# Optimization experiments

Hardware: AMD Instinct MI355X
Metric: run time of the kernel (lower is better)

## Reference

```python
import jax, jax.numpy as jnp
import numpy as np

D = 512          # sequence_dim
H = 8            # num_heads
DA = 64          # attn_dim per head
DV = 64          # linear_dim per head
NB = 4           # num_blocks
N = 1024         # max_seq_length + max_output_len + 1
B = 4
EPS = 1e-6


def setup_inputs() -> dict:
    key = jax.random.key(0)
    ks = jax.random.split(key, 8)
    sequence = jax.random.normal(ks[0], (B, N, D), dtype=jnp.float32)
    sequence_length = jax.random.randint(ks[1], (B,), 1, 1014)
    pos_embed = jax.random.normal(ks[2], (N, D), dtype=jnp.float32)  # nn.Embedding ~ N(0,1)
    w_uvqk = jax.random.normal(ks[3], (NB, D, 2 * H * DV + 2 * H * DA), dtype=jnp.float32) * 0.02
    w_o = jax.random.normal(ks[4], (NB, H * DV, D), dtype=jnp.float32) * 0.02
    b_o = jnp.zeros((NB, D), dtype=jnp.float32)
    ln1_g = jnp.ones((NB, D), dtype=jnp.float32)
    ln1_b = jnp.zeros((NB, D), dtype=jnp.float32)
    ln2_g = jnp.ones((NB, H * DV), dtype=jnp.float32)
    ln2_b = jnp.zeros((NB, H * DV), dtype=jnp.float32)
    pos_w = jax.random.normal(ks[5], (NB, 2 * N - 1), dtype=jnp.float32) * 0.02
    return {
        'sequence': sequence, 'sequence_length': sequence_length,
        'pos_embed': pos_embed, 'ln1_g': ln1_g, 'ln1_b': ln1_b,
        'w_uvqk': w_uvqk, 'ln2_g': ln2_g, 'ln2_b': ln2_b,
        'w_o': w_o, 'b_o': b_o, 'pos_w': pos_w,
    }


def _layer_norm(x, g, b):
    mu = jnp.mean(x, axis=-1, keepdims=True)
    var = jnp.mean(jnp.square(x - mu), axis=-1, keepdims=True)
    return (x - mu) * jax.lax.rsqrt(var + EPS) * g + b


def reference(sequence, sequence_length, pos_embed, ln1_g, ln1_b, w_uvqk,
              ln2_g, ln2_b, w_o, b_o, pos_w):
    # positional embedding + scale (inference: dropout = identity)
    x = sequence * jnp.asarray(np.sqrt(D), sequence.dtype) + pos_embed[None, :, :]
    # length mask (dense-padded equivalent of the jagged representation)
    mask = (jnp.arange(N)[None, :] < sequence_length[:, None]).astype(sequence.dtype)[..., None]
    x = x * mask
    # invalid_attn_mask = 1 - triu(ones, diag=1): causal incl. diagonal
    causal = jnp.tril(jnp.ones((N, N), sequence.dtype))
    # rel_pos_bias[i, j] = pos_w[j - i + N - 1]
    idx = jnp.arange(N)
    rel = idx[None, :] - idx[:, None] + (N - 1)  # (N, N) in [0, 2N-2]
    for l in range(NB):
        nx = _layer_norm(x, ln1_g[l], ln1_b[l])
        uvqk = jax.nn.silu(nx @ w_uvqk[l])  # (B, N, 2*H*DV + 2*H*DA)
        u, v, q, k = jnp.split(uvqk, [H * DV, 2 * H * DV, 2 * H * DV + H * DA], axis=-1)
        qh = q.reshape(x.shape[0], N, H, DA)
        kh = k.reshape(x.shape[0], N, H, DA)
        vh = v.reshape(x.shape[0], N, H, DV)
        qk = jnp.einsum('bnhd,bmhd->bhnm', qh, kh) + pos_w[l][rel][None, None]
        attn = jax.nn.silu(qk) * (causal / N)  # (B, H, N, N)
        av = jnp.einsum('bhnm,bmhd->bnhd', attn, vh).reshape(x.shape[0], N, H * DV)
        o_in = _layer_norm(av, ln2_g[l], ln2_b[l]) * u
        x = (x + o_in @ w_o[l] + b_o[l]) * mask  # mask = dense<->jagged roundtrip
    # output_embeddings[..., :D] then L2-normalize with clamped norm
    norm = jnp.linalg.norm(x, axis=-1, keepdims=True)
    return x / jnp.clip(norm, 1e-6, None)
```

## Files before the change

kernel.cpp:

```cpp
#include <hip/hip_runtime.h>
#include <math.h>
#include <stdint.h>

#define BB 4
#define NN 1024
#define DD 512
#define HH 8
#define ROWS (BB * NN)
#define NBL 4

typedef _Float16 h8 __attribute__((ext_vector_type(8)));
typedef _Float16 h4 __attribute__((ext_vector_type(4)));
typedef _Float16 h2 __attribute__((ext_vector_type(2)));
typedef float f4 __attribute__((ext_vector_type(4)));

__device__ __forceinline__ float fast_silu(float x) {
    float e = __builtin_amdgcn_exp2f(-1.4426950408889634f * x);
    return x * __builtin_amdgcn_rcpf(1.0f + e);
}

__device__ __forceinline__ void gl16(const void* gp, void* lp) {
    __builtin_amdgcn_global_load_lds(
        (const __attribute__((address_space(1))) uint32_t*)gp,
        (__attribute__((address_space(3))) uint32_t*)lp, 16, 0, 0);
}

__global__ __launch_bounds__(256) void k_transpose16(const float* __restrict__ wuvqk,
                                                     _Float16* __restrict__ wuT,
                                                     const float* __restrict__ wo,
                                                     _Float16* __restrict__ woT) {
    __shared__ _Float16 T[64][66];
    int z = blockIdx.z;
    const float* s; _Float16* d; int N;
    if (z < 4) { N = 2048; s = wuvqk + (size_t)z * 512 * 2048; d = wuT + (size_t)z * 2048 * 512; }
    else {
        if (blockIdx.x >= 8) return;
        N = 512; s = wo + (size_t)(z - 4) * 512 * 512; d = woT + (size_t)(z - 4) * 512 * 512;
    }
    int n0 = blockIdx.x << 6, k0 = blockIdx.y << 6;
    int tx = threadIdx.x & 63, ty = threadIdx.x >> 6;
    #pragma unroll
    for (int q = 0; q < 16; ++q)
        T[(q << 2) + ty][tx] = (_Float16)s[(size_t)(k0 + (q << 2) + ty) * N + n0 + tx];
    __syncthreads();
    #pragma unroll
    for (int q = 0; q < 16; ++q)
        d[(size_t)(n0 + (q << 2) + ty) * 512 + k0 + tx] = T[tx][(q << 2) + ty];
}

template<int INIT>
__global__ __launch_bounds__(256) void k_ln(const float* __restrict__ X,
                                            const float* __restrict__ X2,
                                            const float* __restrict__ X3,
                                            const float* __restrict__ seq,
                                            const float* __restrict__ pos,
                                            const int* __restrict__ slen,
                                            const float* __restrict__ g,
                                            const float* __restrict__ bt,
                                            _Float16* __restrict__ O,
                                            const _Float16* __restrict__ U,
                                            float* __restrict__ Xw) {
    __shared__ float sbuf[4];
    int row = blockIdx.x;
    int c = threadIdx.x << 1;
    float2 v;
    if (INIT) {
        int b = row >> 10, n = row & (NN - 1);
        float m = (n < slen[b]) ? 1.0f : 0.0f;
        float2 s2 = *(const float2*)&seq[(size_t)row * 512 + c];
        float2 p2 = *(const float2*)&pos[(size_t)n * 512 + c];
        const float SD = 22.627416997969522f;
        v.x = (s2.x * SD + p2.x) * m;
        v.y = (s2.y * SD + p2.y) * m;
        *(float2*)&Xw[(size_t)row * 512 + c] = v;
    } else {
        v = *(const float2*)&X[(size_t)row * 512 + c];
        int nn = row & 1023;
        if (X2 && nn >= 384) {
            float2 v2 = *(const float2*)&X2[(size_t)row * 512 + c];
            v.x += v2.x; v.y += v2.y;
        }
        if (X3 && nn >= 768) {
            float2 v3 = *(const float2*)&X3[(size_t)row * 512 + c];
            v.x += v3.x; v.y += v3.y;
        }
    }

    float s = v.x + v.y;
    #pragma unroll
    for (int off = 1; off < 64; off <<= 1) s += __shfl_xor(s, off);
    if ((threadIdx.x & 63) == 0) sbuf[threadIdx.x >> 6] = s;
    __syncthreads();
    s = sbuf[0] + sbuf[1] + sbuf[2] + sbuf[3];
    float mu = s * (1.0f / 512.0f);
    float dx = v.x - mu, dy = v.y - mu;
    float ss = dx * dx + dy * dy;
    __syncthreads();
    #pragma unroll
    for (int off = 1; off < 64; off <<= 1) ss += __shfl_xor(ss, off);
    if ((threadIdx.x & 63) == 0) sbuf[threadIdx.x >> 6] = ss;
    __syncthreads();
    ss = sbuf[0] + sbuf[1] + sbuf[2] + sbuf[3];
    float rs = rsqrtf(ss * (1.0f / 512.0f) + 1e-6f);

    float o0 = dx * rs * g[c] + bt[c];
    float o1 = dy * rs * g[c + 1] + bt[c + 1];
    if (U) {
        o0 *= (float)U[(size_t)row * 2048 + c];
        o1 *= (float)U[(size_t)row * 2048 + c + 1];
    }
    h2 o;
    o[0] = (_Float16)o0; o[1] = (_Float16)o1;
    *(h2*)&O[(size_t)row * 512 + c] = o;
}

template<int EPI, int BM, int BN, int WAVES, int WGR, int WGC>
__global__ __launch_bounds__(WAVES * 64) void k_gemm(const _Float16* __restrict__ A,
                                                     const _Float16* __restrict__ Bm,
                                                     int K, int Ncols,
                                                     _Float16* __restrict__ Cu,
                                                     _Float16* __restrict__ vT,
                                                     const float* __restrict__ bo,
                                                     const int* __restrict__ slen,
                                                     float* __restrict__ Xio) {
    constexpr int WR = BM / WGR / 16;
    constexpr int WC = BN / WGC / 16;
    constexpr int QA = BM * 8 / (WAVES * 64);
    constexpr int QB = BN * 8 / (WAVES * 64);
    __shared__ _Float16 As[2][BM * 64];
    __shared__ _Float16 Bs[2][BN * 64];
    int tid = threadIdx.x;
    int w = tid >> 6, lane = tid & 63;
    int t = lane & 15, gq = lane >> 4;
    int flat = blockIdx.y * gridDim.x + blockIdx.x;
    int cpx = (gridDim.x * gridDim.y) >> 3;
    int f2 = (flat & 7) * cpx + (flat >> 3);
    int bx = f2 % gridDim.x, by = f2 / gridDim.x;
    int row0 = by * BM, col0 = bx * BN;
    int wr = (w / WGC) * (BM / WGR), wc = (w % WGC) * (BN / WGC);

    f4 zero4 = {0.0f, 0.0f, 0.0f, 0.0f};
    f4 acc[WR][WC];
    #pragma unroll
    for (int i = 0; i < WR; ++i)
        #pragma unroll
        for (int j = 0; j < WC; ++j) acc[i][j] = zero4;

    auto stage = [&](int buf, int k0) {
        #pragma unroll
        for (int q = 0; q < QA; ++q) {
            int s = (q * WAVES + w) * 64 + lane;
            int r = s >> 3, cs = (s & 7) ^ (r & 7);
            gl16(A + (size_t)(row0 + r) * K + k0 + (cs << 3),
                 (char*)&As[buf][0] + (size_t)(q * WAVES + w) * 1024);
        }
        #pragma unroll
        for (int q = 0; q < QB; ++q) {
            int s = (q * WAVES + w) * 64 + lane;
            int r = s >> 3, cs = (s & 7) ^ (r & 7);
            gl16(Bm + (size_t)(col0 + r) * K + k0 + (cs << 3),
                 (char*)&Bs[buf][0] + (size_t)(q * WAVES + w) * 1024);
        }
    };

    stage(0, 0);
    int cur = 0;
    for (int k0 = 0; k0 < K; k0 += 64) {
        __syncthreads();
        if (k0 + 64 < K) stage(cur ^ 1, k0 + 64);
        h8 af[WR][2], bf[WC][2];
        #pragma unroll
        for (int i = 0; i < WR; ++i) {
            int rl = wr + (i << 4) + t;
            #pragma unroll
            for (int ks = 0; ks < 2; ++ks)
                af[i][ks] = *(const h8*)((const char*)&As[cur][0] + rl * 128 +
                                         (((gq + (ks << 2)) ^ (rl & 7)) << 4));
        }
        #pragma unroll
        for (int j = 0; j < WC; ++j) {
            int nl = wc + (j << 4) + t;
            #pragma unroll
            for (int ks = 0; ks < 2; ++ks)
                bf[j][ks] = *(const h8*)((const char*)&Bs[cur][0] + nl * 128 +
                                         (((gq + (ks << 2)) ^ (nl & 7)) << 4));
        }
        #pragma unroll
        for (int i = 0; i < WR; ++i)
            #pragma unroll
            for (int j = 0; j < WC; ++j) {
                acc[i][j] = __builtin_amdgcn_mfma_f32_16x16x32_f16(af[i][0], bf[j][0], acc[i][j], 0, 0, 0);
                acc[i][j] = __builtin_amdgcn_mfma_f32_16x16x32_f16(af[i][1], bf[j][1], acc[i][j], 0, 0, 0);
            }
        cur ^= 1;
    }

    #pragma unroll
    for (int i = 0; i < WR; ++i) {
        #pragma unroll
        for (int j = 0; j < WC; ++j) {
            int colf = col0 + wc + (j << 4) + t;
            int rowb = row0 + wr + (i << 4) + (gq << 2);
            if (EPI == 0) {
                if (colf >= 512 && colf < 1024) {
                    int b = rowb >> 10;
                    int hh = (colf - 512) >> 6, dd = (colf - 512) & 63;
                    h4 pk;
                    #pragma unroll
                    for (int rr = 0; rr < 4; ++rr) pk[rr] = (_Float16)fast_silu(acc[i][j][rr]);
                    size_t off = ((size_t)((b << 3) + hh) * 64 + dd) * 1024 + (rowb & 1023);
                    *(h4*)&vT[off] = pk;
                } else {
                    #pragma unroll
                    for (int rr = 0; rr < 4; ++rr)
                        Cu[(size_t)(rowb + rr) * 2048 + colf] = (_Float16)fast_silu(acc[i][j][rr]);
                }
            } else {
                int b = rowb >> 10;
                #pragma unroll
                for (int rr = 0; rr < 4; ++rr) {
                    int row = rowb + rr;
                    float m = ((row & 1023) < slen[b]) ? 1.0f : 0.0f;
                    size_t ix = (size_t)row * 512 + colf;
                    Xio[ix] = (Xio[ix] + acc[i][j][rr] + bo[colf]) * m;
                }
            }
        }
    }
}

__global__ __launch_bounds__(256) void k_attn(const _Float16* __restrict__ uvqk,
                                              const _Float16* __restrict__ vT,
                                              const float* __restrict__ posw,
                                              float* __restrict__ av0,
                                              float* __restrict__ av1,
                                              float* __restrict__ av2) {
    __shared__ _Float16 Ks[2][64 * 64];
    __shared__ _Float16 Vs[64 * 64];
    __shared__ _Float16 Ps[64 * 72];
    __shared__ float pws[2][128];
    int tid = threadIdx.x;
    int w = tid >> 6, lane = tid & 63;
    int t = lane & 15, gq = lane >> 4;
    int flat = blockIdx.x + 30 * (blockIdx.y + 8 * blockIdx.z);
    int f2 = (flat & 7) * 120 + (flat >> 3);
    int u = f2 % 30, h = (f2 / 30) & 7, b = f2 / 240;

    int nt, mlo, mhi;
    float* avout;
    if (u < 6) { nt = u; mlo = 0; mhi = nt; avout = av0; }
    else if (u < 18) {
        int p = u - 6; nt = 6 + (p >> 1);
        int c0 = (nt + 2) >> 1;
        if (p & 1) { mlo = c0; mhi = nt; avout = av1; }
        else       { mlo = 0;  mhi = c0 - 1; avout = av0; }
    } else {
        int p = u - 18; int third = p / 3; nt = 12 + third; int q3 = p - 3 * third;
        int c = nt + 1;
        int c1 = (c + 2) / 3, c2 = (2 * c + 2) / 3;
        if (q3 == 0)      { mlo = 0;  mhi = c1 - 1; avout = av0; }
        else if (q3 == 1) { mlo = c1; mhi = c2 - 1; avout = av1; }
        else              { mlo = c2; mhi = nt;     avout = av2; }
    }
    int n0 = nt << 6;

    const _Float16* qbase = uvqk + (size_t)b * NN * 2048 + 1024 + h * 64;
    const _Float16* kbase = uvqk + (size_t)b * NN * 2048 + 1536 + h * 64;
    const _Float16* vbase = vT + (size_t)((b << 3) + h) * 64 * 1024;

    #pragma unroll
    for (int q = 0; q < 2; ++q) {
        int s = (((w << 1) + q) << 6) + lane;
        int r = s >> 3, cs = (s & 7) ^ (r & 7);
        gl16(qbase + (size_t)(n0 + r) * 2048 + (cs << 3),
             (char*)&Ks[1][0] + (size_t)(((w << 1) + q) << 6) * 16);
        gl16(kbase + (size_t)((mlo << 6) + r) * 2048 + (cs << 3),
             (char*)&Ks[0][0] + (size_t)(((w << 1) + q) << 6) * 16);
    }
    if (tid < 128) pws[0][tid] = posw[(mlo << 6) - n0 + tid + 960];
    __syncthreads();

    h8 aq[2];
    {
        int rl = (w << 4) + t;
        #pragma unroll
        for (int ks = 0; ks < 2; ++ks)
            aq[ks] = *(const h8*)((const char*)&Ks[1][0] + rl * 128 +
                                  (((gq + (ks << 2)) ^ (rl & 7)) << 4));
    }
    asm volatile("s_waitcnt lgkmcnt(0)" ::: "memory");
    __builtin_amdgcn_sched_barrier(0);
    __syncthreads();

    f4 zero4 = {0.0f, 0.0f, 0.0f, 0.0f};
    f4 avacc[4];
    #pragma unroll
    for (int j = 0; j < 4; ++j) avacc[j] = zero4;

    int cur = 0;
    for (int mt = mlo; mt <= mhi; ++mt) {
        int m0 = mt << 6;
        #pragma unroll
        for (int q = 0; q < 2; ++q) {
            int s = (((w << 1) + q) << 6) + lane;
            int r = s >> 3, cs = (s & 7) ^ (r & 7);
            gl16(vbase + (size_t)r * 1024 + m0 + (cs << 3),
                 (char*)&Vs[0] + (size_t)(((w << 1) + q) << 6) * 16);
        }
        int mt2 = (mt < mhi) ? mt + 1 : mt;
        #pragma unroll
        for (int q = 0; q < 2; ++q) {
            int s = (((w << 1) + q) << 6) + lane;
            int r = s >> 3, cs = (s & 7) ^ (r & 7);
            gl16(kbase + (size_t)((mt2 << 6) + r) * 2048 + (cs << 3),
                 (char*)&Ks[cur ^ 1][0] + (size_t)(((w << 1) + q) << 6) * 16);
        }
        if (tid < 128) pws[cur ^ 1][tid] = posw[(mt2 << 6) - n0 + tid + 960];

        f4 sacc[4];
        __builtin_amdgcn_s_setprio(1);
        #pragma unroll
        for (int i = 0; i < 4; ++i) {
            f4 binit;
            #pragma unroll
            for (int rr = 0; rr < 4; ++rr)
                binit[rr] = pws[cur][63 + (i << 4) + (gq << 2) + rr - ((w << 4) + t)];
            int ml = (i << 4) + t;
            h8 ak0 = *(const h8*)((const char*)&Ks[cur][0] + ml * 128 + (((gq + 0) ^ (ml & 7)) << 4));
            h8 ak1 = *(const h8*)((const char*)&Ks[cur][0] + ml * 128 + (((gq + 4) ^ (ml & 7)) << 4));
            sacc[i] = __builtin_amdgcn_mfma_f32_16x16x32_f16(ak0, aq[0], binit, 0, 0, 0);
            sacc[i] = __builtin_amdgcn_mfma_f32_16x16x32_f16(ak1, aq[1], sacc[i], 0, 0, 0);
        }
        __builtin_amdgcn_s_setprio(0);
        int nabs = n0 + (w << 4) + t;
        #pragma unroll
        for (int i = 0; i < 4; ++i) {
            int mb = m0 + (i << 4) + (gq << 2);
            h4 pk;
            #pragma unroll
            for (int rr = 0; rr < 4; ++rr) {
                float p = (mb + rr <= nabs) ? fast_silu(sacc[i][rr]) : 0.0f;
                pk[rr] = (_Float16)p;
            }
            *(h4*)((char*)Ps + ((w << 4) + t) * 144 + (i << 5) + (gq << 3)) = pk;
        }
        asm volatile("s_waitcnt lgkmcnt(0)" ::: "memory");
        asm volatile("s_waitcnt vmcnt(2)" ::: "memory");
        __builtin_amdgcn_s_barrier();
        __builtin_amdgcn_s_setprio(1);
        #pragma unroll
        for (int ks = 0; ks < 2; ++ks) {
            h8 pa = *(const h8*)((const char*)Ps + ((w << 4) + t) * 144 + (ks << 6) + (gq << 4));
            #pragma unroll
            for (int jt = 0; jt < 4; ++jt) {
                int dl = (jt << 4) + t;
                h8 bv = *(const h8*)((const char*)&Vs[0] + dl * 128 +
                                     (((gq + (ks << 2)) ^ (dl & 7)) << 4));
                avacc[jt] = __builtin_amdgcn_mfma_f32_16x16x32_f16(pa, bv, avacc[jt], 0, 0, 0);
            }
        }
        __builtin_amdgcn_s_setprio(0);
        __syncthreads();
        cur ^= 1;
    }

    #pragma unroll
    for (int jt = 0; jt < 4; ++jt) {
        #pragma unroll
        for (int rr = 0; rr < 4; ++rr) {
            int n = n0 + (w << 4) + (gq << 2) + rr;
            int d = (jt << 4) + t;
            avout[(size_t)(b * NN + n) * 512 + h * 64 + d] = avacc[jt][rr] * (1.0f / 1024.0f);
        }
    }
}

__global__ __launch_bounds__(256) void k_norm(float* __restrict__ X) {
    __shared__ float sbuf[4];
    int row = blockIdx.x;
    int c = threadIdx.x << 1;
    float2 v = *(const float2*)&X[(size_t)row * 512 + c];
    float ss = v.x * v.x + v.y * v.y;
    #pragma unroll
    for (int off = 1; off < 64; off <<= 1) ss += __shfl_xor(ss, off);
    if ((threadIdx.x & 63) == 0) sbuf[threadIdx.x >> 6] = ss;
    __syncthreads();
    ss = sbuf[0] + sbuf[1] + sbuf[2] + sbuf[3];
    float norm = sqrtf(ss);
    float sc = 1.0f / fmaxf(norm, 1e-6f);
    X[(size_t)row * 512 + c] = v.x * sc;
    X[(size_t)row * 512 + c + 1] = v.y * sc;
}

extern "C" void kernel_launch(void* const* d_in, const int* in_sizes, int n_in,
                              void* d_out, int out_size, void* d_ws, size_t ws_size,
                              hipStream_t stream) {
    const float* seq   = (const float*)d_in[0];
    const int*   slen  = (const int*)d_in[1];
    const float* pos   = (const float*)d_in[2];
    const float* ln1g  = (const float*)d_in[3];
    const float* ln1b  = (const float*)d_in[4];
    const float* wuvqk = (const float*)d_in[5];
    const float* ln2g  = (const float*)d_in[6];
    const float* ln2b  = (const float*)d_in[7];
    const float* wo    = (const float*)d_in[8];
    const float* bo    = (const float*)d_in[9];
    const float* posw  = (const float*)d_in[10];

    float* x = (float*)d_out;
    char* W = (char*)d_ws;
    _Float16* nx16   = (_Float16*)(W);
    _Float16* oin16  = (_Float16*)(W + (4u << 20));
    _Float16* uvqk16 = (_Float16*)(W + (8u << 20));
    _Float16* vT16   = (_Float16*)(W + (24u << 20));
    float*    av0    = (float*)   (W + (28u << 20));
    float*    av1    = (float*)   (W + (36u << 20));
    float*    av2    = (float*)   (W + (44u << 20));
    _Float16* wuT16  = (_Float16*)(W + (52u << 20));
    _Float16* woT16  = (_Float16*)(W + (60u << 20));

    k_transpose16<<<dim3(32, 8, 8), 256, 0, stream>>>(wuvqk, wuT16, wo, woT16);
    for (int l = 0; l < NBL; ++l) {
        if (l == 0)
            k_ln<1><<<ROWS, 256, 0, stream>>>(nullptr, nullptr, nullptr, seq, pos, slen,
                                              ln1g, ln1b, nx16, nullptr, x);
        else
            k_ln<0><<<ROWS, 256, 0, stream>>>(x, nullptr, nullptr, nullptr, nullptr, nullptr,
                                              ln1g + l * 512, ln1b + l * 512, nx16, nullptr, nullptr);
        k_gemm<0, 128, 128, 8, 2, 4><<<dim3(16, 32), 512, 0, stream>>>(
            nx16, wuT16 + (size_t)l * 2048 * 512, 512, 2048, uvqk16, vT16, nullptr, nullptr, nullptr);
        k_attn<<<dim3(30, 8, NBL), 256, 0, stream>>>(uvqk16, vT16, posw + l * (2 * NN - 1),
                                                     av0, av1, av2);
        k_ln<0><<<ROWS, 256, 0, stream>>>(av0, av1, av2, nullptr, nullptr, nullptr,
                                          ln2g + l * 512, ln2b + l * 512, oin16, uvqk16, nullptr);
        k_gemm<1, 64, 32, 4, 2, 2><<<dim3(16, 64), 256, 0, stream>>>(
            oin16, woT16 + (size_t)l * 512 * 512, 512, 512, nullptr, nullptr, bo + l * 512, slen, x);
    }
    k_norm<<<ROWS, 256, 0, stream>>>(x);
}
```

Before: 234.7 us.

## Use wave-per-row layernorm/norm kernels and LDS-staged coalesced GEMM epilogue stores

The layernorm and final L2-norm kernels now give each wave two full rows, using 8-wide vector loads and shuffle-only reductions with no LDS or block barriers, and launch 512 blocks instead of 4096. The UVQK GEMM epilogue now writes SiLU outputs into shared memory first, then emits coalesced 16-byte stores for both the row-major uvqk buffer and the transposed V buffer, replacing scattered 2-byte and strided h4 stores. K is hardcoded to 512 in the GEMM. The epilogue adds an extra LDS round-trip and barriers.

New measurement: 208.7 us, median of 2. 11.1% less time.

```diff
diff --git a/kernel.cpp b/kernel.cpp
--- a/kernel.cpp
+++ b/kernel.cpp
@@ -2,16 +2,12 @@
 #include <math.h>
 #include <stdint.h>
 
-#define BB 4
 #define NN 1024
-#define DD 512
-#define HH 8
-#define ROWS (BB * NN)
+#define ROWS 4096
 #define NBL 4
 
 typedef _Float16 h8 __attribute__((ext_vector_type(8)));
 typedef _Float16 h4 __attribute__((ext_vector_type(4)));
-typedef _Float16 h2 __attribute__((ext_vector_type(2)));
 typedef float f4 __attribute__((ext_vector_type(4)));
 
 __device__ __forceinline__ float fast_silu(float x) {
@@ -23,6 +19,12 @@
     __builtin_amdgcn_global_load_lds(
         (const __attribute__((address_space(1))) uint32_t*)gp,
         (__attribute__((address_space(3))) uint32_t*)lp, 16, 0, 0);
+}
+
+__device__ __forceinline__ float wred(float s) {
+    #pragma unroll
+    for (int off = 1; off < 64; off <<= 1) s += __shfl_xor(s, off);
+    return s;
 }
 
 __global__ __launch_bounds__(256) void k_transpose16(const float* __restrict__ wuvqk,
@@ -48,76 +50,109 @@
         d[(size_t)(n0 + (q << 2) + ty) * 512 + k0 + tx] = T[tx][(q << 2) + ty];
 }
 
-template<int INIT>
-__global__ __launch_bounds__(256) void k_ln(const float* __restrict__ X,
-                                            const float* __restrict__ X2,
-                                            const float* __restrict__ X3,
-                                            const float* __restrict__ seq,
-                                            const float* __restrict__ pos,
-                                            const int* __restrict__ slen,
-                                            const float* __restrict__ g,
-                                            const float* __restrict__ bt,
-                                            _Float16* __restrict__ O,
-                                            const _Float16* __restrict__ U,
-                                            float* __restrict__ Xw) {
-    __shared__ float sbuf[4];
-    int row = blockIdx.x;
-    int c = threadIdx.x << 1;
-    float2 v;
-    if (INIT) {
-        int b = row >> 10, n = row & (NN - 1);
-        float m = (n < slen[b]) ? 1.0f : 0.0f;
-        float2 s2 = *(const float2*)&seq[(size_t)row * 512 + c];
-        float2 p2 = *(const float2*)&pos[(size_t)n * 512 + c];
-        const float SD = 22.627416997969522f;
-        v.x = (s2.x * SD + p2.x) * m;
-        v.y = (s2.y * SD + p2.y) * m;
-        *(float2*)&Xw[(size_t)row * 512 + c] = v;
-    } else {
-        v = *(const float2*)&X[(size_t)row * 512 + c];
-        int nn = row & 1023;
-        if (X2 && nn >= 384) {
-            float2 v2 = *(const float2*)&X2[(size_t)row * 512 + c];
-            v.x += v2.x; v.y += v2.y;
-        }
-        if (X3 && nn >= 768) {
-            float2 v3 = *(const float2*)&X3[(size_t)row * 512 + c];
-            v.x += v3.x; v.y += v3.y;
-        }
-    }
-
-    float s = v.x + v.y;
-    #pragma unroll
-    for (int off = 1; off < 64; off <<= 1) s += __shfl_xor(s, off);
-    if ((threadIdx.x & 63) == 0) sbuf[threadIdx.x >> 6] = s;
-    __syncthreads();
-    s = sbuf[0] + sbuf[1] + sbuf[2] + sbuf[3];
-    float mu = s * (1.0f / 512.0f);
-    float dx = v.x - mu, dy = v.y - mu;
-    float ss = dx * dx + dy * dy;
-    __syncthreads();
-    #pragma unroll
-    for (int off = 1; off < 64; off <<= 1) ss += __shfl_xor(ss, off);
-    if ((threadIdx.x & 63) == 0) sbuf[threadIdx.x >> 6] = ss;
-    __syncthreads();
-    ss = sbuf[0] + sbuf[1] + sbuf[2] + sbuf[3];
-    float rs = rsqrtf(ss * (1.0f / 512.0f) + 1e-6f);
-
-    float o0 = dx * rs * g[c] + bt[c];
-    float o1 = dy * rs * g[c + 1] + bt[c + 1];
-    if (U) {
-        o0 *= (float)U[(size_t)row * 2048 + c];
-        o1 *= (float)U[(size_t)row * 2048 + c + 1];
-    }
-    h2 o;
-    o[0] = (_Float16)o0; o[1] = (_Float16)o1;
-    *(h2*)&O[(size_t)row * 512 + c] = o;
+template<int MODE>
+__global__ __launch_bounds__(256) void k_lnw(const float* __restrict__ X,
+                                             const float* __restrict__ X2,
+                                             const float* __restrict__ X3,
+                                             const float* __restrict__ seq,
+                                             const float* __restrict__ pos,
+                                             const int* __restrict__ slen,
+                                             const float* __restrict__ g,
+                                             const float* __restrict__ bt,
+                                             _Float16* __restrict__ O,
+                                             const _Float16* __restrict__ U,
+                                             float* __restrict__ Xw) {
+    int tid = threadIdx.x;
+    int w = tid >> 6, lane = tid & 63;
+    int c = lane << 3;
+    #pragma unroll
+    for (int rr = 0; rr < 2; ++rr) {
+        int row = (blockIdx.x << 3) + (w << 1) + rr;
+        float v[8];
+        if (MODE == 1) {
+            int b = row >> 10, n = row & (NN - 1);
+            float m = (n < slen[b]) ? 1.0f : 0.0f;
+            const float4* sp = (const float4*)&seq[(size_t)row * 512 + c];
+            const float4* pp = (const float4*)&pos[(size_t)n * 512 + c];
+            const float SD = 22.627416997969522f;
+            float4 s0 = sp[0], s1 = sp[1], p0 = pp[0], p1 = pp[1];
+            v[0]=(s0.x*SD+p0.x)*m; v[1]=(s0.y*SD+p0.y)*m; v[2]=(s0.z*SD+p0.z)*m; v[3]=(s0.w*SD+p0.w)*m;
+            v[4]=(s1.x*SD+p1.x)*m; v[5]=(s1.y*SD+p1.y)*m; v[6]=(s1.z*SD+p1.z)*m; v[7]=(s1.w*SD+p1.w)*m;
+            float4 o0, o1;
+            o0.x=v[0]; o0.y=v[1]; o0.z=v[2]; o0.w=v[3];
+            o1.x=v[4]; o1.y=v[5]; o1.z=v[6]; o1.w=v[7];
+            float4* xp = (float4*)&Xw[(size_t)row * 512 + c];
+            xp[0] = o0; xp[1] = o1;
+        } else {
+            const float4* xp = (const float4*)&X[(size_t)row * 512 + c];
+            float4 a = xp[0], b4 = xp[1];
+            v[0]=a.x; v[1]=a.y; v[2]=a.z; v[3]=a.w; v[4]=b4.x; v[5]=b4.y; v[6]=b4.z; v[7]=b4.w;
+            if (MODE == 2) {
+                int nn = row & (NN - 1);
+                if (nn >= 384) {
+                    const float4* qp = (const float4*)&X2[(size_t)row * 512 + c];
+                    float4 t0 = qp[0], t1 = qp[1];
+                    v[0]+=t0.x; v[1]+=t0.y; v[2]+=t0.z; v[3]+=t0.w;
+                    v[4]+=t1.x; v[5]+=t1.y; v[6]+=t1.z; v[7]+=t1.w;
+                }
+                if (nn >= 768) {
+                    const float4* qp = (const float4*)&X3[(size_t)row * 512 + c];
+                    float4 t0 = qp[0], t1 = qp[1];
+                    v[0]+=t0.x; v[1]+=t0.y; v[2]+=t0.z; v[3]+=t0.w;
+                    v[4]+=t1.x; v[5]+=t1.y; v[6]+=t1.z; v[7]+=t1.w;
+                }
+            }
+        }
+        float s = v[0]+v[1]+v[2]+v[3]+v[4]+v[5]+v[6]+v[7];
+        s = wred(s);
+        float mu = s * (1.0f / 512.0f);
+        float ss = 0.0f;
+        #pragma unroll
+        for (int i = 0; i < 8; ++i) { float d = v[i] - mu; ss += d * d; }
+        ss = wred(ss);
+        float rs = rsqrtf(ss * (1.0f / 512.0f) + 1e-6f);
+
+        const float4* gp = (const float4*)&g[c];
+        const float4* bp = (const float4*)&bt[c];
+        float4 g0 = gp[0], g1 = gp[1], b0 = bp[0], b1 = bp[1];
+        float gg[8] = {g0.x,g0.y,g0.z,g0.w,g1.x,g1.y,g1.z,g1.w};
+        float bb[8] = {b0.x,b0.y,b0.z,b0.w,b1.x,b1.y,b1.z,b1.w};
+        float o[8];
+        #pragma unroll
+        for (int i = 0; i < 8; ++i) o[i] = (v[i] - mu) * rs * gg[i] + bb[i];
+        if (MODE == 2) {
+            h8 uu = *(const h8*)&U[(size_t)row * 2048 + c];
+            #pragma unroll
+            for (int i = 0; i < 8; ++i) o[i] *= (float)uu[i];
+        }
+        h8 oh;
+        #pragma unroll
+        for (int i = 0; i < 8; ++i) oh[i] = (_Float16)o[i];
+        *(h8*)&O[(size_t)row * 512 + c] = oh;
+    }
+}
+
+__global__ __launch_bounds__(256) void k_normw(float* __restrict__ X) {
+    int tid = threadIdx.x;
+    int w = tid >> 6, lane = tid & 63;
+    int c = lane << 3;
+    #pragma unroll
+    for (int rr = 0; rr < 2; ++rr) {
+        int row = (blockIdx.x << 3) + (w << 1) + rr;
+        float4* xp = (float4*)&X[(size_t)row * 512 + c];
+        float4 a = xp[0], b4 = xp[1];
+        float ss = a.x*a.x + a.y*a.y + a.z*a.z + a.w*a.w +
+                   b4.x*b4.x + b4.y*b4.y + b4.z*b4.z + b4.w*b4.w;
+        ss = wred(ss);
+        float sc = 1.0f / fmaxf(sqrtf(ss), 1e-6f);
+        a.x*=sc; a.y*=sc; a.z*=sc; a.w*=sc; b4.x*=sc; b4.y*=sc; b4.z*=sc; b4.w*=sc;
+        xp[0] = a; xp[1] = b4;
+    }
 }
 
 template<int EPI, int BM, int BN, int WAVES, int WGR, int WGC>
 __global__ __launch_bounds__(WAVES * 64) void k_gemm(const _Float16* __restrict__ A,
                                                      const _Float16* __restrict__ Bm,
-                                                     int K, int Ncols,
                                                      _Float16* __restrict__ Cu,
                                                      _Float16* __restrict__ vT,
                                                      const float* __restrict__ bo,
@@ -127,8 +162,9 @@
     constexpr int WC = BN / WGC / 16;
     constexpr int QA = BM * 8 / (WAVES * 64);
     constexpr int QB = BN * 8 / (WAVES * 64);
-    __shared__ _Float16 As[2][BM * 64];
-    __shared__ _Float16 Bs[2][BN * 64];
+    __shared__ _Float16 smem[2 * 64 * (BM + BN)];
+    _Float16* AsB = smem;
+    _Float16* BsB = smem + 2 * BM * 64;
     int tid = threadIdx.x;
     int w = tid >> 6, lane = tid & 63;
     int t = lane & 15, gq = lane >> 4;
@@ -147,43 +183,45 @@
         for (int j = 0; j < WC; ++j) acc[i][j] = zero4;
 
     auto stage = [&](int buf, int k0) {
+        _Float16* As = AsB + buf * BM * 64;
+        _Float16* Bs = BsB + buf * BN * 64;
         #pragma unroll
         for (int q = 0; q < QA; ++q) {
             int s = (q * WAVES + w) * 64 + lane;
             int r = s >> 3, cs = (s & 7) ^ (r & 7);
-            gl16(A + (size_t)(row0 + r) * K + k0 + (cs << 3),
-                 (char*)&As[buf][0] + (size_t)(q * WAVES + w) * 1024);
+            gl16(A + (size_t)(row0 + r) * 512 + k0 + (cs << 3),
+                 (char*)As + (size_t)(q * WAVES + w) * 1024);
         }
         #pragma unroll
         for (int q = 0; q < QB; ++q) {
             int s = (q * WAVES + w) * 64 + lane;
             int r = s >> 3, cs = (s & 7) ^ (r & 7);
-            gl16(Bm + (size_t)(col0 + r) * K + k0 + (cs << 3),
-                 (char*)&Bs[buf][0] + (size_t)(q * WAVES + w) * 1024);
+            gl16(Bm + (size_t)(col0 + r) * 512 + k0 + (cs << 3),
+                 (char*)Bs + (size_t)(q * WAVES + w) * 1024);
         }
     };
 
     stage(0, 0);
     int cur = 0;
-    for (int k0 = 0; k0 < K; k0 += 64) {
+    for (int k0 = 0; k0 < 512; k0 += 64) {
         __syncthreads();
-        if (k0 + 64 < K) stage(cur ^ 1, k0 + 64);
+        if (k0 + 64 < 512) stage(cur ^ 1, k0 + 64);
+        const char* As = (const char*)(AsB + cur * BM * 64);
+        const char* Bs = (const char*)(BsB + cur * BN * 64);
         h8 af[WR][2], bf[WC][2];
         #pragma unroll
         for (int i = 0; i < WR; ++i) {
             int rl = wr + (i << 4) + t;
             #pragma unroll
             for (int ks = 0; ks < 2; ++ks)
-                af[i][ks] = *(const h8*)((const char*)&As[cur][0] + rl * 128 +
-                                         (((gq + (ks << 2)) ^ (rl & 7)) << 4));
+                af[i][ks] = *(const h8*)(As + rl * 128 + (((gq + (ks << 2)) ^ (rl & 7)) << 4));
         }
         #pragma unroll
         for (int j = 0; j < WC; ++j) {
             int nl = wc + (j << 4) + t;
             #pragma unroll
             for (int ks = 0; ks < 2; ++ks)
-                bf[j][ks] = *(const h8*)((const char*)&Bs[cur][0] + nl * 128 +
-                                         (((gq + (ks << 2)) ^ (nl & 7)) << 4));
+                bf[j][ks] = *(const h8*)(Bs + nl * 128 + (((gq + (ks << 2)) ^ (nl & 7)) << 4));
         }
         #pragma unroll
         for (int i = 0; i < WR; ++i)
@@ -195,27 +233,63 @@
         cur ^= 1;
     }
 
-    #pragma unroll
-    for (int i = 0; i < WR; ++i) {
-        #pragma unroll
-        for (int j = 0; j < WC; ++j) {
-            int colf = col0 + wc + (j << 4) + t;
-            int rowb = row0 + wr + (i << 4) + (gq << 2);
-            if (EPI == 0) {
-                if (colf >= 512 && colf < 1024) {
-                    int b = rowb >> 10;
-                    int hh = (colf - 512) >> 6, dd = (colf - 512) & 63;
+    if (EPI == 0) {
+        _Float16* E = smem;
+        bool vblk = (col0 >= 512 && col0 < 1024);
+        __syncthreads();
+        if (vblk) {
+            #pragma unroll
+            for (int i = 0; i < WR; ++i)
+                #pragma unroll
+                for (int j = 0; j < WC; ++j) {
+                    int cl = wc + (j << 4) + t;
+                    int rl = wr + (i << 4) + (gq << 2);
                     h4 pk;
                     #pragma unroll
                     for (int rr = 0; rr < 4; ++rr) pk[rr] = (_Float16)fast_silu(acc[i][j][rr]);
-                    size_t off = ((size_t)((b << 3) + hh) * 64 + dd) * 1024 + (rowb & 1023);
-                    *(h4*)&vT[off] = pk;
-                } else {
+                    *(h4*)&E[cl * 136 + rl] = pk;
+                }
+        } else {
+            #pragma unroll
+            for (int i = 0; i < WR; ++i)
+                #pragma unroll
+                for (int j = 0; j < WC; ++j) {
+                    int cl = wc + (j << 4) + t;
+                    int rl = wr + (i << 4) + (gq << 2);
                     #pragma unroll
                     for (int rr = 0; rr < 4; ++rr)
-                        Cu[(size_t)(rowb + rr) * 2048 + colf] = (_Float16)fast_silu(acc[i][j][rr]);
+                        E[(rl + rr) * 136 + cl] = (_Float16)fast_silu(acc[i][j][rr]);
                 }
-            } else {
+        }
+        __syncthreads();
+        constexpr int ITERS = 128 * 16 / (WAVES * 64);
+        if (vblk) {
+            int b = row0 >> 10;
+            int n0l = row0 & 1023;
+            #pragma unroll
+            for (int it = 0; it < ITERS; ++it) {
+                int dl = it * (WAVES * 4) + (tid >> 4);
+                int cc = tid & 15;
+                h8 vv = *(const h8*)&E[dl * 136 + (cc << 3)];
+                int hh = (col0 + dl - 512) >> 6, dd = (col0 + dl - 512) & 63;
+                *(h8*)&vT[((size_t)((b << 3) + hh) * 64 + dd) * 1024 + n0l + (cc << 3)] = vv;
+            }
+        } else {
+            #pragma unroll
+            for (int it = 0; it < ITERS; ++it) {
+                int rl = it * (WAVES * 4) + (tid >> 4);
+                int cc = tid & 15;
+                h8 vv = *(const h8*)&E[rl * 136 + (cc << 3)];
+                *(h8*)&Cu[(size_t)(row0 + rl) * 2048 + col0 + (cc << 3)] = vv;
+            }
+        }
+    } else {
+        #pragma unroll
+        for (int i = 0; i < WR; ++i) {
+            #pragma unroll
+            for (int j = 0; j < WC; ++j) {
+                int colf = col0 + wc + (j << 4) + t;
+                int rowb = row0 + wr + (i << 4) + (gq << 2);
                 int b = rowb >> 10;
                 #pragma unroll
                 for (int rr = 0; rr < 4; ++rr) {
@@ -256,8 +330,7 @@
         else       { mlo = 0;  mhi = c0 - 1; avout = av0; }
     } else {
         int p = u - 18; int third = p / 3; nt = 12 + third; int q3 = p - 3 * third;
-        int c = nt + 1;
-        int c1 = (c + 2) / 3, c2 = (2 * c + 2) / 3;
+        int c = nt + 1, c1 = (c + 2) / 3, c2 = (2 * c + 2) / 3;
         if (q3 == 0)      { mlo = 0;  mhi = c1 - 1; avout = av0; }
         else if (q3 == 1) { mlo = c1; mhi = c2 - 1; avout = av1; }
         else              { mlo = c2; mhi = nt;     avout = av2; }
@@ -373,23 +446,6 @@
             avout[(size_t)(b * NN + n) * 512 + h * 64 + d] = avacc[jt][rr] * (1.0f / 1024.0f);
         }
     }
-}
-
-__global__ __launch_bounds__(256) void k_norm(float* __restrict__ X) {
-    __shared__ float sbuf[4];
-    int row = blockIdx.x;
-    int c = threadIdx.x << 1;
-    float2 v = *(const float2*)&X[(size_t)row * 512 + c];
-    float ss = v.x * v.x + v.y * v.y;
-    #pragma unroll
-    for (int off = 1; off < 64; off <<= 1) ss += __shfl_xor(ss, off);
-    if ((threadIdx.x & 63) == 0) sbuf[threadIdx.x >> 6] = ss;
-    __syncthreads();
-    ss = sbuf[0] + sbuf[1] + sbuf[2] + sbuf[3];
-    float norm = sqrtf(ss);
-    float sc = 1.0f / fmaxf(norm, 1e-6f);
-    X[(size_t)row * 512 + c] = v.x * sc;
-    X[(size_t)row * 512 + c + 1] = v.y * sc;
 }
 
 extern "C" void kernel_launch(void* const* d_in, const int* in_sizes, int n_in,
@@ -422,19 +478,19 @@
     k_transpose16<<<dim3(32, 8, 8), 256, 0, stream>>>(wuvqk, wuT16, wo, woT16);
     for (int l = 0; l < NBL; ++l) {
         if (l == 0)
-            k_ln<1><<<ROWS, 256, 0, stream>>>(nullptr, nullptr, nullptr, seq, pos, slen,
+            k_lnw<1><<<512, 256, 0, stream>>>(nullptr, nullptr, nullptr, seq, pos, slen,
                                               ln1g, ln1b, nx16, nullptr, x);
         else
-            k_ln<0><<<ROWS, 256, 0, stream>>>(x, nullptr, nullptr, nullptr, nullptr, nullptr,
+            k_lnw<0><<<512, 256, 0, stream>>>(x, nullptr, nullptr, nullptr, nullptr, nullptr,
                                               ln1g + l * 512, ln1b + l * 512, nx16, nullptr, nullptr);
         k_gemm<0, 128, 128, 8, 2, 4><<<dim3(16, 32), 512, 0, stream>>>(
-            nx16, wuT16 + (size_t)l * 2048 * 512, 512, 2048, uvqk16, vT16, nullptr, nullptr, nullptr);
+            nx16, wuT16 + (size_t)l * 2048 * 512, uvqk16, vT16, nullptr, nullptr, nullptr);
         k_attn<<<dim3(30, 8, NBL), 256, 0, stream>>>(uvqk16, vT16, posw + l * (2 * NN - 1),
                                                      av0, av1, av2);
-        k_ln<0><<<ROWS, 256, 0, stream>>>(av0, av1, av2, nullptr, nullptr, nullptr,
+        k_lnw<2><<<512, 256, 0, stream>>>(av0, av1, av2, nullptr, nullptr, nullptr,
                                           ln2g + l * 512, ln2b + l * 512, oin16, uvqk16, nullptr);
         k_gemm<1, 64, 32, 4, 2, 2><<<dim3(16, 64), 256, 0, stream>>>(
-            oin16, woT16 + (size_t)l * 512 * 512, 512, 512, nullptr, nullptr, bo + l * 512, slen, x);
-    }
-    k_norm<<<ROWS, 256, 0, stream>>>(x);
-}
+            oin16, woT16 + (size_t)l * 512 * 512, nullptr, nullptr, bo + l * 512, slen, x);
+    }
+    k_normw<<<512, 256, 0, stream>>>(x);
+}
```
